# Kernel tuning notes

Hardware: AMD Instinct MI355X
Metric: run time of the kernel (lower is better)

## Reference

```python
import jax, jax.numpy as jnp
import numpy as np

NUM_EXPERTS = 64
TOP_K = 2

def setup_inputs() -> dict:
    key = jax.random.key(0)
    k1, k2, k3, k4 = jax.random.split(key, 4)
    B, N, C, E = 4, 4096, 2048, NUM_EXPERTS
    x = jax.random.normal(k1, (B, N, C), dtype=jnp.float32)
    routing_context = jax.random.normal(k2, (B, C), dtype=jnp.float32)
    # Linear(C, E, bias=False) and Linear(C, C, bias=False), torch layout (out, in)
    gate_w = jax.random.normal(k3, (E, C), dtype=jnp.float32) * (1.0 / np.sqrt(C))
    ctx_w = jax.random.normal(k4, (C, C), dtype=jnp.float32) * (1.0 / np.sqrt(C))
    return {"x": x, "routing_context": routing_context, "gate_w": gate_w, "ctx_w": ctx_w}

def reference(x, routing_context, gate_w, ctx_w):
    B, N, C = x.shape
    T = B * N
    E = gate_w.shape[0]
    # context_proj(routing_context): (B,C) @ (C,C)^T -> broadcast over N
    ctx = routing_context @ ctx_w.T                      # (B, C)
    x_routing = (x + ctx[:, None, :]).reshape(T, C)      # (T, C)
    logits = x_routing @ gate_w.T                        # (T, E)
    top_vals, top_idx = jax.lax.top_k(logits, TOP_K)     # (T, K) each
    top_weights = jax.nn.softmax(top_vals, axis=-1)      # (T, K)
    probs = jax.nn.softmax(logits, axis=-1)              # (T, E)
    importance = probs.sum(axis=0) / T                   # (E,)
    # load: fraction of tokens that pick each expert in their top-k
    load = jnp.zeros((E,), dtype=probs.dtype).at[top_idx.reshape(-1)].add(1.0) / T
    aux_loss = E * (importance * load).sum()
    return top_idx, top_weights, aux_loss
```

## Files before the change

### kernel.cpp

```cpp
#include <hip/hip_runtime.h>
#include <math.h>

#define T_TOKENS 16384
#define C_DIM    2048
#define N_SEQ    4096
#define E_EXP    64
#define NSLICE   4
#define KSLICE   512
#define EPB      1024
#define GN       131072

typedef __attribute__((ext_vector_type(8))) short  short8;
typedef __attribute__((ext_vector_type(4))) float  floatx4;

__device__ __forceinline__ void splitv(float v, ushort& h, ushort& m, ushort& l) {
    unsigned u = __float_as_uint(v);
    h = (ushort)(u >> 16);
    float f1 = v - __uint_as_float(u & 0xffff0000u);
    unsigned u1 = __float_as_uint(f1);
    m = (ushort)(u1 >> 16);
    float f2 = f1 - __uint_as_float(u1 & 0xffff0000u);
    l = (ushort)(__float_as_uint(f2) >> 16);
}

__device__ __forceinline__ void splitpack8(const float4& a, const float4& b,
                                           short8& h, short8& m, short8& l) {
    ushort hh, mm, ll;
    splitv(a.x, hh, mm, ll); h[0] = hh; m[0] = mm; l[0] = ll;
    splitv(a.y, hh, mm, ll); h[1] = hh; m[1] = mm; l[1] = ll;
    splitv(a.z, hh, mm, ll); h[2] = hh; m[2] = mm; l[2] = ll;
    splitv(a.w, hh, mm, ll); h[3] = hh; m[3] = mm; l[3] = ll;
    splitv(b.x, hh, mm, ll); h[4] = hh; m[4] = mm; l[4] = ll;
    splitv(b.y, hh, mm, ll); h[5] = hh; m[5] = mm; l[5] = ll;
    splitv(b.z, hh, mm, ll); h[6] = hh; m[6] = mm; l[6] = ll;
    splitv(b.w, hh, mm, ll); h[7] = hh; m[7] = mm; l[7] = ll;
}

__device__ __forceinline__ void split3rne(float v, ushort& h, ushort& m, ushort& l) {
    unsigned u = __float_as_uint(v);
    unsigned r = (u + 0x7fffu + ((u >> 16) & 1u)) >> 16;
    h = (ushort)r;
    float e1 = v - __uint_as_float(r << 16);
    u = __float_as_uint(e1);
    r = (u + 0x7fffu + ((u >> 16) & 1u)) >> 16;
    m = (ushort)r;
    float e2 = e1 - __uint_as_float(r << 16);
    l = (ushort)(__float_as_uint(e2) >> 16);
}

__device__ __forceinline__ void ctx_body(
    int j, int lane, const float* __restrict__ rc,
    const float* __restrict__ ctx_w, float* __restrict__ ctx_out)
{
    const float4* wr = (const float4*)(ctx_w + (size_t)j * C_DIM);
    const float4* r0 = (const float4*)(rc);
    const float4* r1 = (const float4*)(rc + C_DIM);
    const float4* r2 = (const float4*)(rc + 2 * C_DIM);
    const float4* r3 = (const float4*)(rc + 3 * C_DIM);

    float s0 = 0.f, s1 = 0.f, s2 = 0.f, s3 = 0.f;
#pragma unroll
    for (int it = 0; it < 8; ++it) {
        float4 a  = wr[it * 64 + lane];
        float4 c0 = r0[it * 64 + lane];
        float4 c1 = r1[it * 64 + lane];
        float4 c2 = r2[it * 64 + lane];
        float4 c3 = r3[it * 64 + lane];
        s0 += a.x * c0.x + a.y * c0.y + a.z * c0.z + a.w * c0.w;
        s1 += a.x * c1.x + a.y * c1.y + a.z * c1.z + a.w * c1.w;
        s2 += a.x * c2.x + a.y * c2.y + a.z * c2.z + a.w * c2.w;
        s3 += a.x * c3.x + a.y * c3.y + a.z * c3.z + a.w * c3.w;
    }
#pragma unroll
    for (int off = 32; off; off >>= 1) {
        s0 += __shfl_xor(s0, off, 64);
        s1 += __shfl_xor(s1, off, 64);
        s2 += __shfl_xor(s2, off, 64);
        s3 += __shfl_xor(s3, off, 64);
    }
    if (lane == 0) {
        ctx_out[j]             = s0;
        ctx_out[C_DIM + j]     = s1;
        ctx_out[2 * C_DIM + j] = s2;
        ctx_out[3 * C_DIM + j] = s3;
    }
}

__global__ __launch_bounds__(256) void split_kernel(
    const float* __restrict__ gw, ushort* __restrict__ gsp)
{
    const int idx  = blockIdx.x * 256 + threadIdx.x;
    const int j    = idx & 7;
    const int e    = (idx >> 3) & 63;
    const int koct = idx >> 9;
    float g = gw[(size_t)e * C_DIM + koct * 8 + j];
    ushort h, m, l;
    split3rne(g, h, m, l);
    gsp[idx]          = h;
    gsp[GN + idx]     = m;
    gsp[2 * GN + idx] = l;
}

__global__ __launch_bounds__(256, 2) void gemm_ctx_kernel(
    const float* __restrict__ x, const ushort* __restrict__ gsp,
    const float* __restrict__ rc, const float* __restrict__ ctx_w,
    float* __restrict__ ctx_out, float* __restrict__ P)
{
    if (blockIdx.x >= 128 * NSLICE) {
        const int lane = threadIdx.x & 63;
        const int j = (blockIdx.x - 128 * NSLICE) * 4 + (threadIdx.x >> 6);
        ctx_body(j, lane, rc, ctx_w, ctx_out);
        return;
    }

    const int tid   = threadIdx.x;
    const int wv    = tid >> 6;
    const int lane  = tid & 63;
    const int l15   = lane & 15;
    const int quad  = lane >> 4;
    const int tile  = blockIdx.x & 127;
    const int slice = blockIdx.x >> 7;
    const int tw    = tile * 128 + wv * 32;
    const int cbase = slice * KSLICE;

    floatx4 acc[2][4];
#pragma unroll
    for (int s = 0; s < 2; ++s)
#pragma unroll
        for (int nt = 0; nt < 4; ++nt) acc[s][nt] = (floatx4){0.f, 0.f, 0.f, 0.f};

    const float* xr0 = x + (size_t)(tw + l15) * C_DIM + cbase + quad * 8;
    const float* xr1 = xr0 + (size_t)16 * C_DIM;
    const ushort* bb = gsp + ((size_t)((cbase >> 3) + quad) * 64 + l15) * 8;

    const int NKS = KSLICE / 32;

    float4 a00 = *(const float4*)(xr0);
    float4 a01 = *(const float4*)(xr0 + 4);
    float4 a10 = *(const float4*)(xr1);
    float4 a11 = *(const float4*)(xr1 + 4);

#pragma unroll 2
    for (int ks = 0; ks < NKS; ++ks) {
        const int nk = (ks + 1 < NKS) ? (ks + 1) : 0;
        float4 n00 = *(const float4*)(xr0 + nk * 32);
        float4 n01 = *(const float4*)(xr0 + nk * 32 + 4);
        float4 n10 = *(const float4*)(xr1 + nk * 32);
        float4 n11 = *(const float4*)(xr1 + nk * 32 + 4);

        const ushort* bks = bb + (size_t)ks * 4 * 64 * 8;
        short8 bh[4], bm[4], bl[4];
#pragma unroll
        for (int nt = 0; nt < 4; ++nt) {
            const ushort* bp_ = bks + (size_t)(16 * nt) * 8;
            bh[nt] = *(const short8*)(bp_);
            bm[nt] = *(const short8*)(bp_ + GN);
            bl[nt] = *(const short8*)(bp_ + 2 * (size_t)GN);
        }

        short8 ah0, am0, al0, ah1, am1, al1;
        splitpack8(a00, a01, ah0, am0, al0);
        splitpack8(a10, a11, ah1, am1, al1);

#pragma unroll
        for (int nt = 0; nt < 4; ++nt) {
            acc[0][nt] = __builtin_amdgcn_mfma_f32_16x16x32_bf16(ah0, bh[nt], acc[0][nt], 0, 0, 0);
            acc[0][nt] = __builtin_amdgcn_mfma_f32_16x16x32_bf16(ah0, bm[nt], acc[0][nt], 0, 0, 0);
            acc[0][nt] = __builtin_amdgcn_mfma_f32_16x16x32_bf16(am0, bh[nt], acc[0][nt], 0, 0, 0);
            acc[0][nt] = __builtin_amdgcn_mfma_f32_16x16x32_bf16(ah0, bl[nt], acc[0][nt], 0, 0, 0);
            acc[0][nt] = __builtin_amdgcn_mfma_f32_16x16x32_bf16(al0, bh[nt], acc[0][nt], 0, 0, 0);
            acc[0][nt] = __builtin_amdgcn_mfma_f32_16x16x32_bf16(am0, bm[nt], acc[0][nt], 0, 0, 0);
            acc[1][nt] = __builtin_amdgcn_mfma_f32_16x16x32_bf16(ah1, bh[nt], acc[1][nt], 0, 0, 0);
            acc[1][nt] = __builtin_amdgcn_mfma_f32_16x16x32_bf16(ah1, bm[nt], acc[1][nt], 0, 0, 0);
            acc[1][nt] = __builtin_amdgcn_mfma_f32_16x16x32_bf16(am1, bh[nt], acc[1][nt], 0, 0, 0);
            acc[1][nt] = __builtin_amdgcn_mfma_f32_16x16x32_bf16(ah1, bl[nt], acc[1][nt], 0, 0, 0);
            acc[1][nt] = __builtin_amdgcn_mfma_f32_16x16x32_bf16(al1, bh[nt], acc[1][nt], 0, 0, 0);
            acc[1][nt] = __builtin_amdgcn_mfma_f32_16x16x32_bf16(am1, bm[nt], acc[1][nt], 0, 0, 0);
        }

        a00 = n00; a01 = n01; a10 = n10; a11 = n11;
    }

    float* Ps = P + ((size_t)slice * T_TOKENS + tw) * E_EXP;
#pragma unroll
    for (int s = 0; s < 2; ++s)
#pragma unroll
        for (int nt = 0; nt < 4; ++nt)
#pragma unroll
            for (int r = 0; r < 4; ++r)
                Ps[(size_t)(s * 16 + quad * 4 + r) * E_EXP + 16 * nt + l15] =
                    acc[s][nt][r];
}

__global__ __launch_bounds__(256) void cl_kernel(
    const float* __restrict__ gw, const float* __restrict__ ctx,
    float* __restrict__ cl)
{
    const int lane = threadIdx.x & 63;
    const int pk   = blockIdx.x * 4 + (threadIdx.x >> 6);
    const int b    = pk >> 6;
    const int e    = pk & 63;
    const float4* wr = (const float4*)(gw + (size_t)e * C_DIM);
    const float4* cr = (const float4*)(ctx + (size_t)b * C_DIM);
    float s = 0.f;
#pragma unroll
    for (int it = 0; it < 8; ++it) {
        float4 a = wr[it * 64 + lane];
        float4 c = cr[it * 64 + lane];
        s += a.x * c.x + a.y * c.y + a.z * c.z + a.w * c.w;
    }
#pragma unroll
    for (int off = 32; off; off >>= 1) s += __shfl_xor(s, off, 64);
    if (lane == 0) cl[pk] = s;
}

__global__ __launch_bounds__(256) void epilogue_kernel(
    const float* __restrict__ P, const float* __restrict__ cl,
    float* __restrict__ out, float* __restrict__ bp)
{
    __shared__ float red[4][128];

    const int tid  = threadIdx.x;
    const int wv   = tid >> 6;
    const int lane = tid & 63;
    const int t0   = blockIdx.x * (T_TOKENS / EPB);
    const float clv = cl[(t0 >> 12) * 64 + lane];

    float imp_acc = 0.f, cnt_acc = 0.f;

    for (int tt = 0; tt < 4; ++tt) {
        const int t = t0 + wv * 4 + tt;
        float v = clv;
#pragma unroll
        for (int s = 0; s < NSLICE; ++s)
            v += P[((size_t)s * T_TOKENS + t) * E_EXP + lane];

        const float p = expf(v);
        float v1 = v;  int i1 = lane;
        float v2 = -INFINITY; int i2 = 0x7fffffff;
        float s = p;
#pragma unroll
        for (int off = 32; off; off >>= 1) {
            float ov1 = __shfl_xor(v1, off, 64);
            int   oi1 = __shfl_xor(i1, off, 64);
            float ov2 = __shfl_xor(v2, off, 64);
            int   oi2 = __shfl_xor(i2, off, 64);
            s += __shfl_xor(s, off, 64);
            const bool aw = (ov1 < v1) || (ov1 == v1 && i1 < oi1);
            const float lv = aw ? ov1 : v1;  const int li = aw ? oi1 : i1;
            const float wv2 = aw ? v2 : ov2; const int wi = aw ? i2 : oi2;
            if (!aw) { v1 = ov1; i1 = oi1; }
            const bool sw = (wv2 < lv) || (wv2 == lv && li < wi);
            v2 = sw ? lv : wv2; i2 = sw ? li : wi;
        }

        imp_acc += p / s;
        if (lane == i1 || lane == i2) cnt_acc += 1.f;

        if (lane == 0) {
            const float e2 = expf(v2 - v1);
            out[2 * t]     = (float)i1;
            out[2 * t + 1] = (float)i2;
            out[2 * T_TOKENS + 2 * t]     = 1.f / (1.f + e2);
            out[2 * T_TOKENS + 2 * t + 1] = e2 / (1.f + e2);
        }
    }

    red[wv][lane]      = imp_acc;
    red[wv][64 + lane] = cnt_acc;
    __syncthreads();
    if (tid < 128) {
        float s = red[0][tid] + red[1][tid] + red[2][tid] + red[3][tid];
        bp[(size_t)blockIdx.x * 128 + tid] = s;
    }
}

__global__ __launch_bounds__(1024) void aux_kernel(
    const float* __restrict__ bp, int nb, float* __restrict__ out_aux)
{
    __shared__ float4 red[32][32];
    const int tid = threadIdx.x;
    const int c4  = tid & 31;
    const int grp = tid >> 5;

    const float4* bp4 = (const float4*)bp;
    float4 s = make_float4(0.f, 0.f, 0.f, 0.f);
    for (int r = grp; r < nb; r += 32) {
        float4 v = bp4[(size_t)r * 32 + c4];
        s.x += v.x; s.y += v.y; s.z += v.z; s.w += v.w;
    }
    red[grp][c4] = s;
    __syncthreads();

    if (tid < 32) {
        float4 t = make_float4(0.f, 0.f, 0.f, 0.f);
#pragma unroll
        for (int g = 0; g < 32; ++g) {
            float4 v = red[g][tid];
            t.x += v.x; t.y += v.y; t.z += v.z; t.w += v.w;
        }
        red[0][tid] = t;
    }
    __syncthreads();

    if (tid < 16) {
        float4 a = red[0][tid];
        float4 b = red[0][tid + 16];
        float v = a.x * b.x + a.y * b.y + a.z * b.z + a.w * b.w;
#pragma unroll
        for (int off = 8; off; off >>= 1) v += __shfl_xor(v, off, 64);
        if (tid == 0)
            out_aux[0] = (float)E_EXP * v / ((float)T_TOKENS * (float)T_TOKENS);
    }
}

__global__ __launch_bounds__(256) void ctx_only_kernel(
    const float* __restrict__ rc, const float* __restrict__ ctx_w,
    float* __restrict__ ctx_out)
{
    const int lane = threadIdx.x & 63;
    const int j    = blockIdx.x * 4 + (threadIdx.x >> 6);
    ctx_body(j, lane, rc, ctx_w, ctx_out);
}

#define TM    64
#define FKC   64
#define FLSTR 68
__global__ __launch_bounds__(256) void router_fused_kernel(
    const float* __restrict__ x, const float* __restrict__ gate_w,
    const float* __restrict__ ctx, float* __restrict__ out,
    float* __restrict__ bp)
{
    __shared__ float xs[TM][FLSTR];
    __shared__ float gs[E_EXP][FLSTR];
    __shared__ float ls[TM][FLSTR];
    __shared__ float red[4][128];

    const int tid = threadIdx.x;
    const int eg  = tid & 15;
    const int tg  = tid >> 4;
    const int t0  = blockIdx.x * TM;
    const int b   = t0 / N_SEQ;
    const int sr  = tid >> 4;
    const int scg = tid & 15;
    const float* ctx_row = ctx + (size_t)b * C_DIM;

    float4 acc[4][4];
#pragma unroll
    for (int i = 0; i < 4; ++i)
#pragma unroll
        for (int j = 0; j < 4; ++j) acc[i][j] = make_float4(0.f, 0.f, 0.f, 0.f);

    float4 px[4], pg[4], pc;
    auto prefetch = [&](int kc) {
        const int c0 = kc * FKC + scg * 4;
        pc = *(const float4*)(ctx_row + c0);
#pragma unroll
        for (int i = 0; i < 4; ++i) {
            px[i] = *(const float4*)(x + (size_t)(t0 + sr + 16 * i) * C_DIM + c0);
            pg[i] = *(const float4*)(gate_w + (size_t)(sr + 16 * i) * C_DIM + c0);
        }
    };

    prefetch(0);
    const int NCHUNK = C_DIM / FKC;
    for (int kc = 0; kc < NCHUNK; ++kc) {
        __syncthreads();
#pragma unroll
        for (int i = 0; i < 4; ++i) {
            float4 v = px[i];
            v.x += pc.x; v.y += pc.y; v.z += pc.z; v.w += pc.w;
            *(float4*)&xs[sr + 16 * i][scg * 4] = v;
            *(float4*)&gs[sr + 16 * i][scg * 4] = pg[i];
        }
        __syncthreads();
        if (kc + 1 < NCHUNK) prefetch(kc + 1);
#pragma unroll
        for (int cc = 0; cc < FKC; cc += 4) {
            float4 xv[4], gv[4];
#pragma unroll
            for (int i = 0; i < 4; ++i) xv[i] = *(const float4*)&xs[tg + 16 * i][cc];
#pragma unroll
            for (int j = 0; j < 4; ++j) gv[j] = *(const float4*)&gs[eg + 16 * j][cc];
#pragma unroll
            for (int i = 0; i < 4; ++i)
#pragma unroll
                for (int j = 0; j < 4; ++j) {
                    acc[i][j].x = fmaf(xv[i].x, gv[j].x, acc[i][j].x);
                    acc[i][j].y = fmaf(xv[i].y, gv[j].y, acc[i][j].y);
                    acc[i][j].z = fmaf(xv[i].z, gv[j].z, acc[i][j].z);
                    acc[i][j].w = fmaf(xv[i].w, gv[j].w, acc[i][j].w);
                }
        }
    }

    __syncthreads();
#pragma unroll
    for (int i = 0; i < 4; ++i)
#pragma unroll
        for (int j = 0; j < 4; ++j)
            ls[tg + 16 * i][eg + 16 * j] =
                (acc[i][j].x + acc[i][j].y) + (acc[i][j].z + acc[i][j].w);
    __syncthreads();

    const int wv   = tid >> 6;
    const int lane = tid & 63;
    float imp_acc = 0.f, cnt_acc = 0.f;

    for (int tt = 0; tt < 16; ++tt) {
        const int tokL = wv * 16 + tt;
        const float v = ls[tokL][lane];
        const float p = expf(v);
        float v1 = v;  int i1 = lane;
        float v2 = -INFINITY; int i2 = 0x7fffffff;
        float s = p;
#pragma unroll
        for (int off = 32; off; off >>= 1) {
            float ov1 = __shfl_xor(v1, off, 64);
            int   oi1 = __shfl_xor(i1, off, 64);
            float ov2 = __shfl_xor(v2, off, 64);
            int   oi2 = __shfl_xor(i2, off, 64);
            s += __shfl_xor(s, off, 64);
            const bool aw = (ov1 < v1) || (ov1 == v1 && i1 < oi1);
            const float lv = aw ? ov1 : v1;  const int li = aw ? oi1 : i1;
            const float wv2 = aw ? v2 : ov2; const int wi = aw ? i2 : oi2;
            if (!aw) { v1 = ov1; i1 = oi1; }
            const bool sw = (wv2 < lv) || (wv2 == lv && li < wi);
            v2 = sw ? lv : wv2; i2 = sw ? li : wi;
        }
        imp_acc += p / s;
        if (lane == i1 || lane == i2) cnt_acc += 1.f;
        if (lane == 0) {
            const int t = t0 + tokL;
            const float e2 = expf(v2 - v1);
            out[2 * t]     = (float)i1;
            out[2 * t + 1] = (float)i2;
            out[2 * T_TOKENS + 2 * t]     = 1.f / (1.f + e2);
            out[2 * T_TOKENS + 2 * t + 1] = e2 / (1.f + e2);
        }
    }

    red[wv][lane]      = imp_acc;
    red[wv][64 + lane] = cnt_acc;
    __syncthreads();
    if (tid < 128) {
        float s = red[0][tid] + red[1][tid] + red[2][tid] + red[3][tid];
        bp[(size_t)blockIdx.x * 128 + tid] = s;
    }
}

extern "C" void kernel_launch(void* const* d_in, const int* in_sizes, int n_in,
                              void* d_out, int out_size, void* d_ws, size_t ws_size,
                              hipStream_t stream)
{
    (void)in_sizes; (void)n_in; (void)out_size;
    const float* x      = (const float*)d_in[0];
    const float* rc     = (const float*)d_in[1];
    const float* gate_w = (const float*)d_in[2];
    const float* ctx_w  = (const float*)d_in[3];
    float* out = (float*)d_out;

    float*  ctx = (float*)d_ws;
    float*  cl  = ctx + 8192;
    float*  bp  = cl + 256;
    float*  P   = bp + (size_t)EPB * 128;
    ushort* gsp = (ushort*)(P + (size_t)NSLICE * T_TOKENS * E_EXP);

    const size_t need =
        (8192 + 256 + (size_t)EPB * 128 + (size_t)NSLICE * T_TOKENS * E_EXP)
            * sizeof(float)
        + (size_t)3 * GN * sizeof(ushort);

    if (ws_size >= need) {
        split_kernel<<<512, 256, 0, stream>>>(gate_w, gsp);
        gemm_ctx_kernel<<<128 * NSLICE + 512, 256, 0, stream>>>(
            x, gsp, rc, ctx_w, ctx, P);
        cl_kernel<<<64, 256, 0, stream>>>(gate_w, ctx, cl);
        epilogue_kernel<<<EPB, 256, 0, stream>>>(P, cl, out, bp);
        aux_kernel<<<1, 1024, 0, stream>>>(bp, EPB, out + 2 * 2 * T_TOKENS);
    } else {
        ctx_only_kernel<<<512, 256, 0, stream>>>(rc, ctx_w, ctx);
        router_fused_kernel<<<256, 256, 0, stream>>>(x, gate_w, ctx, out, bp);
        aux_kernel<<<1, 1024, 0, stream>>>(bp, 256, out + 2 * 2 * T_TOKENS);
    }
}
```

Before: 245.8 us.

## Stage gate-weight split tiles in double-buffered LDS shared across waves

Each block now loads the three bf16 split planes of the gate weights for each K step once, cooperatively, into a double-buffered XOR-swizzled LDS tile. Previously every wave fetched the same B fragments from global memory on its own. The global loads for the next step are issued into registers before the current step's MFMAs, which overlaps them with compute. This removes redundant global/L2 traffic for B, at the cost of a __syncthreads per step, extra LDS reads, and 24KB of shared memory that could affect occupancy.

```diff
diff --git a/kernel.cpp b/kernel.cpp
--- a/kernel.cpp
+++ b/kernel.cpp
@@ -106,6 +106,8 @@
     const float* __restrict__ rc, const float* __restrict__ ctx_w,
     float* __restrict__ ctx_out, float* __restrict__ P)
 {
+    __shared__ ushort Bs[2][3][2048];
+
     if (blockIdx.x >= 128 * NSLICE) {
         const int lane = threadIdx.x & 63;
         const int j = (blockIdx.x - 128 * NSLICE) * 4 + (threadIdx.x >> 6);
@@ -131,10 +133,20 @@
 
     const float* xr0 = x + (size_t)(tw + l15) * C_DIM + cbase + quad * 8;
     const float* xr1 = xr0 + (size_t)16 * C_DIM;
-    const ushort* bb = gsp + ((size_t)((cbase >> 3) + quad) * 64 + l15) * 8;
+
+    const int swsrc = (tid * 8) ^ (((tid >> 6) & 3) << 3);
+    const size_t stepbase0 = (size_t)(cbase >> 3) * 512;
+
+    int roff[4];
+#pragma unroll
+    for (int nt = 0; nt < 4; ++nt)
+        roff[nt] = quad * 512 + (((16 * nt + l15) ^ quad) << 3);
 
     const int NKS = KSLICE / 32;
 
+    short8 bn0 = *(const short8*)(gsp + 0 * (size_t)GN + stepbase0 + swsrc);
+    short8 bn1 = *(const short8*)(gsp + 1 * (size_t)GN + stepbase0 + swsrc);
+    short8 bn2 = *(const short8*)(gsp + 2 * (size_t)GN + stepbase0 + swsrc);
     float4 a00 = *(const float4*)(xr0);
     float4 a01 = *(const float4*)(xr0 + 4);
     float4 a10 = *(const float4*)(xr1);
@@ -142,40 +154,45 @@
 
 #pragma unroll 2
     for (int ks = 0; ks < NKS; ++ks) {
+        ushort* bw = &Bs[ks & 1][0][0];
+        *(short8*)(bw + 0 * 2048 + tid * 8) = bn0;
+        *(short8*)(bw + 1 * 2048 + tid * 8) = bn1;
+        *(short8*)(bw + 2 * 2048 + tid * 8) = bn2;
+
         const int nk = (ks + 1 < NKS) ? (ks + 1) : 0;
+        const size_t sb = stepbase0 + (size_t)nk * 2048;
+        bn0 = *(const short8*)(gsp + 0 * (size_t)GN + sb + swsrc);
+        bn1 = *(const short8*)(gsp + 1 * (size_t)GN + sb + swsrc);
+        bn2 = *(const short8*)(gsp + 2 * (size_t)GN + sb + swsrc);
         float4 n00 = *(const float4*)(xr0 + nk * 32);
         float4 n01 = *(const float4*)(xr0 + nk * 32 + 4);
         float4 n10 = *(const float4*)(xr1 + nk * 32);
         float4 n11 = *(const float4*)(xr1 + nk * 32 + 4);
 
-        const ushort* bks = bb + (size_t)ks * 4 * 64 * 8;
-        short8 bh[4], bm[4], bl[4];
-#pragma unroll
-        for (int nt = 0; nt < 4; ++nt) {
-            const ushort* bp_ = bks + (size_t)(16 * nt) * 8;
-            bh[nt] = *(const short8*)(bp_);
-            bm[nt] = *(const short8*)(bp_ + GN);
-            bl[nt] = *(const short8*)(bp_ + 2 * (size_t)GN);
-        }
-
         short8 ah0, am0, al0, ah1, am1, al1;
         splitpack8(a00, a01, ah0, am0, al0);
         splitpack8(a10, a11, ah1, am1, al1);
 
+        __syncthreads();
+
+        const ushort* br = &Bs[ks & 1][0][0];
 #pragma unroll
         for (int nt = 0; nt < 4; ++nt) {
-            acc[0][nt] = __builtin_amdgcn_mfma_f32_16x16x32_bf16(ah0, bh[nt], acc[0][nt], 0, 0, 0);
-            acc[0][nt] = __builtin_amdgcn_mfma_f32_16x16x32_bf16(ah0, bm[nt], acc[0][nt], 0, 0, 0);
-            acc[0][nt] = __builtin_amdgcn_mfma_f32_16x16x32_bf16(am0, bh[nt], acc[0][nt], 0, 0, 0);
-            acc[0][nt] = __builtin_amdgcn_mfma_f32_16x16x32_bf16(ah0, bl[nt], acc[0][nt], 0, 0, 0);
-            acc[0][nt] = __builtin_amdgcn_mfma_f32_16x16x32_bf16(al0, bh[nt], acc[0][nt], 0, 0, 0);
-            acc[0][nt] = __builtin_amdgcn_mfma_f32_16x16x32_bf16(am0, bm[nt], acc[0][nt], 0, 0, 0);
-            acc[1][nt] = __builtin_amdgcn_mfma_f32_16x16x32_bf16(ah1, bh[nt], acc[1][nt], 0, 0, 0);
-            acc[1][nt] = __builtin_amdgcn_mfma_f32_16x16x32_bf16(ah1, bm[nt], acc[1][nt], 0, 0, 0);
-            acc[1][nt] = __builtin_amdgcn_mfma_f32_16x16x32_bf16(am1, bh[nt], acc[1][nt], 0, 0, 0);
-            acc[1][nt] = __builtin_amdgcn_mfma_f32_16x16x32_bf16(ah1, bl[nt], acc[1][nt], 0, 0, 0);
-            acc[1][nt] = __builtin_amdgcn_mfma_f32_16x16x32_bf16(al1, bh[nt], acc[1][nt], 0, 0, 0);
-            acc[1][nt] = __builtin_amdgcn_mfma_f32_16x16x32_bf16(am1, bm[nt], acc[1][nt], 0, 0, 0);
+            short8 bh = *(const short8*)(br + 0 * 2048 + roff[nt]);
+            short8 bm = *(const short8*)(br + 1 * 2048 + roff[nt]);
+            short8 bl = *(const short8*)(br + 2 * 2048 + roff[nt]);
+            acc[0][nt] = __builtin_amdgcn_mfma_f32_16x16x32_bf16(ah0, bh, acc[0][nt], 0, 0, 0);
+            acc[0][nt] = __builtin_amdgcn_mfma_f32_16x16x32_bf16(ah0, bm, acc[0][nt], 0, 0, 0);
+            acc[0][nt] = __builtin_amdgcn_mfma_f32_16x16x32_bf16(am0, bh, acc[0][nt], 0, 0, 0);
+            acc[0][nt] = __builtin_amdgcn_mfma_f32_16x16x32_bf16(ah0, bl, acc[0][nt], 0, 0, 0);
+            acc[0][nt] = __builtin_amdgcn_mfma_f32_16x16x32_bf16(al0, bh, acc[0][nt], 0, 0, 0);
+            acc[0][nt] = __builtin_amdgcn_mfma_f32_16x16x32_bf16(am0, bm, acc[0][nt], 0, 0, 0);
+            acc[1][nt] = __builtin_amdgcn_mfma_f32_16x16x32_bf16(ah1, bh, acc[1][nt], 0, 0, 0);
+            acc[1][nt] = __builtin_amdgcn_mfma_f32_16x16x32_bf16(ah1, bm, acc[1][nt], 0, 0, 0);
+            acc[1][nt] = __builtin_amdgcn_mfma_f32_16x16x32_bf16(am1, bh, acc[1][nt], 0, 0, 0);
+            acc[1][nt] = __builtin_amdgcn_mfma_f32_16x16x32_bf16(ah1, bl, acc[1][nt], 0, 0, 0);
+            acc[1][nt] = __builtin_amdgcn_mfma_f32_16x16x32_bf16(al1, bh, acc[1][nt], 0, 0, 0);
+            acc[1][nt] = __builtin_amdgcn_mfma_f32_16x16x32_bf16(am1, bm, acc[1][nt], 0, 0, 0);
         }
 
         a00 = n00; a01 = n01; a10 = n10; a11 = n11;
```

Result: faster. 240.9 us (-2.0%).
